# Kernel tuning notes

Hardware: AMD Instinct MI355X
Metric: run time of the kernel (lower is better)

The kernel has to match this reference:

```python
import jax, jax.numpy as jnp
import numpy as np

N = 65536   # number of feature vectors (feat_num)
D = 512     # feature dim (feat_size)
NC = 256    # number of unique classes n; N % NC == 0 as required by feat.chunk(n, 0)
EPS = 1e-8  # torch nn.CosineSimilarity eps


def setup_inputs() -> dict:
    key = jax.random.key(0)
    feat = jax.random.normal(key, (N, D), dtype=jnp.float32)
    # contiguous class blocks so chunk(n,0) groups match unique labels (module's implicit assumption)
    label = (jnp.arange(N, dtype=jnp.int32) // (N // NC)).astype(jnp.int32)
    return {"feat": feat, "label": label}


def reference(feat, label):
    n = NC  # len(label.unique()); static by construction
    # per-class centers: mean of each contiguous chunk  -> [n, D]
    centers = feat.reshape(n, N // n, D).mean(axis=1)
    # pairwise cosine similarity (torch CosineSimilarity: dot / (max(|x|,eps)*max(|y|,eps)))
    norms = jnp.sqrt(jnp.sum(centers * centers, axis=1, keepdims=True))  # [n,1]
    normed = centers / jnp.maximum(norms, EPS)
    sim = normed @ normed.T  # [n, n]
    # mask = label1 eq label1^T; labels are unique -> identity mask. Off-diagonal min per row.
    eye = jnp.eye(n, dtype=bool)
    dist_an = jnp.min(jnp.where(eye, jnp.inf, sim), axis=1)  # [n]
    # sum_i (1 - min_j!=i sim[i,j])
    return jnp.sum(1.0 - dist_an)
```

## Files before the change

kernel.cpp:

```cpp
#include <hip/hip_runtime.h>
#include <math.h>

#define NFEAT 65536
#define DIM   512
#define D4    128
#define NCLS  256
#define ROWS_PER_CLASS 256
#define EPSV  1e-8f

__global__ __launch_bounds__(1024)
void kA_center_norm(const float4* __restrict__ feat4, float4* __restrict__ nT4,
                    float* __restrict__ out) {
    const int cls  = blockIdx.x;
    const int t    = threadIdx.x;
    const int col4 = t & 127;
    const int sub  = t >> 7;
    const int row0 = cls * ROWS_PER_CLASS + sub * 32;

    const float4* p = feat4 + (size_t)row0 * D4 + col4;
    float4 acc = make_float4(0.f, 0.f, 0.f, 0.f);
#pragma unroll 8
    for (int r = 0; r < 32; ++r) {
        float4 v = p[(size_t)r * D4];
        acc.x += v.x; acc.y += v.y; acc.z += v.z; acc.w += v.w;
    }

    __shared__ float4 red[1024];
    red[t] = acc;
    __syncthreads();

    __shared__ float wsum[2];
    __shared__ float s_inv;
    float4 c = make_float4(0.f, 0.f, 0.f, 0.f);
    if (t < 128) {
        c = red[t];
#pragma unroll
        for (int s = 1; s < 8; ++s) {
            float4 v = red[t + 128 * s];
            c.x += v.x; c.y += v.y; c.z += v.z; c.w += v.w;
        }
        const float ms = 1.0f / (float)ROWS_PER_CLASS;
        c.x *= ms; c.y *= ms; c.z *= ms; c.w *= ms;

        float ss = c.x*c.x + c.y*c.y + c.z*c.z + c.w*c.w;
#pragma unroll
        for (int o = 32; o > 0; o >>= 1) ss += __shfl_down(ss, o, 64);
        if ((t & 63) == 0) wsum[t >> 6] = ss;
    }
    __syncthreads();
    if (t == 0) {
        float nrm = sqrtf(wsum[0] + wsum[1]);
        s_inv = 1.0f / fmaxf(nrm, EPSV);
        if (cls == 0) out[0] = 0.f;
    }
    __syncthreads();
    if (t < 128) {
        const float inv = s_inv;
        c.x *= inv; c.y *= inv; c.z *= inv; c.w *= inv;
        nT4[(size_t)col4 * NCLS + cls] = c;
    }
}

__global__ __launch_bounds__(256)
void kB_min_sum(const float4* __restrict__ nT4, float* __restrict__ out) {
    const int j = blockIdx.x;
    const int i = threadIdx.x;

    __shared__ float4 bj[D4];
    if (i < D4) bj[i] = nT4[(size_t)i * NCLS + j];
    __syncthreads();

    float acc = 0.f;
#pragma unroll 8
    for (int g = 0; g < D4; ++g) {
        float4 a = nT4[(size_t)g * NCLS + i];
        float4 b = bj[g];
        acc += a.x*b.x + a.y*b.y + a.z*b.z + a.w*b.w;
    }
    if (i == j) acc = INFINITY;

#pragma unroll
    for (int o = 32; o > 0; o >>= 1) acc = fminf(acc, __shfl_down(acc, o, 64));

    __shared__ float wmin[4];
    if ((i & 63) == 0) wmin[i >> 6] = acc;
    __syncthreads();
    if (i == 0) {
        float m = fminf(fminf(wmin[0], wmin[1]), fminf(wmin[2], wmin[3]));
        atomicAdd(out, 1.0f - m);
    }
}

extern "C" void kernel_launch(void* const* d_in, const int* in_sizes, int n_in,
                              void* d_out, int out_size, void* d_ws, size_t ws_size,
                              hipStream_t stream) {
    const float* feat = (const float*)d_in[0];
    float* out = (float*)d_out;

    float* nT4f = (float*)d_ws;

    kA_center_norm <<<NCLS, 1024, 0, stream>>>((const float4*)feat, (float4*)nT4f, out);
    kB_min_sum     <<<NCLS,  256, 0, stream>>>((const float4*)nT4f, out);
}
```

Measured before the change: 198.2 us.

## Fuse center/normalize and min-sum kernels with a global grid barrier

Merges the two kernels into one launch, separating the centering/normalizing phase from the pairwise similarity min phase with a software grid barrier built on device-scope atomic counters. The second phase now splits the dot product across all 1024 threads in four partial sums reduced through shared memory. This removes a kernel launch boundary and tail gap. It relies on all 256 blocks being co-resident; otherwise it deadlocks.

After: 221.1 us. +11.5%, slower.

```diff
diff --git a/kernel.cpp b/kernel.cpp
--- a/kernel.cpp
+++ b/kernel.cpp
@@ -8,11 +8,15 @@
 #define ROWS_PER_CLASS 256
 #define EPSV  1e-8f
 
+__device__ int g_arrive = 0;
+__device__ int g_depart = 0;
+
 __global__ __launch_bounds__(1024)
-void kA_center_norm(const float4* __restrict__ feat4, float4* __restrict__ nT4,
-                    float* __restrict__ out) {
+void k_fused(const float4* __restrict__ feat4, float4* __restrict__ nT4,
+             float* __restrict__ out) {
     const int cls  = blockIdx.x;
     const int t    = threadIdx.x;
+
     const int col4 = t & 127;
     const int sub  = t >> 7;
     const int row0 = cls * ROWS_PER_CLASS + sub * 32;
@@ -59,35 +63,59 @@
         c.x *= inv; c.y *= inv; c.z *= inv; c.w *= inv;
         nT4[(size_t)col4 * NCLS + cls] = c;
     }
-}
 
-__global__ __launch_bounds__(256)
-void kB_min_sum(const float4* __restrict__ nT4, float* __restrict__ out) {
-    const int j = blockIdx.x;
-    const int i = threadIdx.x;
-
-    __shared__ float4 bj[D4];
-    if (i < D4) bj[i] = nT4[(size_t)i * NCLS + j];
+    __syncthreads();
+    if (t == 0) {
+        __threadfence();
+        __hip_atomic_fetch_add(&g_arrive, 1, __ATOMIC_RELEASE,
+                               __HIP_MEMORY_SCOPE_AGENT);
+        while (__hip_atomic_load(&g_arrive, __ATOMIC_RELAXED,
+                                 __HIP_MEMORY_SCOPE_AGENT) < NCLS)
+            __builtin_amdgcn_s_sleep(2);
+        __threadfence();
+    }
     __syncthreads();
 
-    float acc = 0.f;
+    const int j = cls;
+    __shared__ float4 bj[D4];
+    __shared__ float  pacc[4][256];
+    __shared__ float  wmin[4];
+    if (t < D4) bj[t] = nT4[(size_t)t * NCLS + j];
+    __syncthreads();
+
+    const int i    = t & 255;
+    const int part = t >> 8;
+    const int g0   = part * 32;
+    float dacc = 0.f;
 #pragma unroll 8
-    for (int g = 0; g < D4; ++g) {
+    for (int g = g0; g < g0 + 32; ++g) {
         float4 a = nT4[(size_t)g * NCLS + i];
         float4 b = bj[g];
-        acc += a.x*b.x + a.y*b.y + a.z*b.z + a.w*b.w;
+        dacc += a.x*b.x + a.y*b.y + a.z*b.z + a.w*b.w;
     }
-    if (i == j) acc = INFINITY;
+    pacc[part][i] = dacc;
+    __syncthreads();
 
+    if (t < 256) {
+        float d = pacc[0][i] + pacc[1][i] + pacc[2][i] + pacc[3][i];
+        if (i == j) d = INFINITY;
 #pragma unroll
-    for (int o = 32; o > 0; o >>= 1) acc = fminf(acc, __shfl_down(acc, o, 64));
-
-    __shared__ float wmin[4];
-    if ((i & 63) == 0) wmin[i >> 6] = acc;
+        for (int o = 32; o > 0; o >>= 1) d = fminf(d, __shfl_down(d, o, 64));
+        if ((i & 63) == 0) wmin[i >> 6] = d;
+    }
     __syncthreads();
-    if (i == 0) {
+    if (t == 0) {
         float m = fminf(fminf(wmin[0], wmin[1]), fminf(wmin[2], wmin[3]));
         atomicAdd(out, 1.0f - m);
+
+        int old = __hip_atomic_fetch_add(&g_depart, 1, __ATOMIC_ACQ_REL,
+                                         __HIP_MEMORY_SCOPE_AGENT);
+        if (old == NCLS - 1) {
+            __hip_atomic_store(&g_arrive, 0, __ATOMIC_RELAXED,
+                               __HIP_MEMORY_SCOPE_AGENT);
+            __hip_atomic_store(&g_depart, 0, __ATOMIC_RELAXED,
+                               __HIP_MEMORY_SCOPE_AGENT);
+        }
     }
 }
 
@@ -99,6 +127,5 @@
 
     float* nT4f = (float*)d_ws;
 
-    kA_center_norm <<<NCLS, 1024, 0, stream>>>((const float4*)feat, (float4*)nT4f, out);
-    kB_min_sum     <<<NCLS,  256, 0, stream>>>((const float4*)nT4f, out);
+    k_fused<<<NCLS, 1024, 0, stream>>>((const float4*)feat, (float4*)nT4f, out);
 }
```
